# Kernel tuning notes

Hardware: AMD Instinct MI355X
Metric: run time of the kernel (lower is better)

## Reference

```python
import jax, jax.numpy as jnp
import numpy as np

EPS = 1e-4

def _softmax_kernel(x, proj, is_query):
    # x: [b,h,n,d], proj: [m,d]
    d = x.shape[-1]
    m = proj.shape[0]
    data_norm = 1.0 / d ** 0.25
    ratio = 1.0 / m ** 0.5
    xd = jnp.einsum('bhnd,md->bhnm', data_norm * x, proj)  # [b,h,n,m]
    diag = jnp.sum(x * x, axis=-1, keepdims=True) * (0.5 * data_norm ** 2)  # [b,h,n,1]
    if is_query:
        stab = jnp.max(xd, axis=-1, keepdims=True)  # per-row max
    else:
        stab = jnp.max(xd)  # global max, matches torch.max(data_dash)
    return ratio * (jnp.exp(xd - diag - stab) + EPS)

def setup_inputs() -> dict:
    key = jax.random.key(0)
    kq, kk, kv, kp = jax.random.split(key, 4)
    B, H, N, D, M = 4, 16, 4096, 64, 256
    return {
        'q': jax.random.normal(kq, (B, H, N, D), dtype=jnp.float32),
        'k': jax.random.normal(kk, (B, H, N, D), dtype=jnp.float32),
        'v': jax.random.normal(kv, (B, H, N, D), dtype=jnp.float32),
        'proj': jax.random.normal(kp, (M, D), dtype=jnp.float32),
    }

def reference(q, k, v, proj):
    q_kernel = _softmax_kernel(q, proj, is_query=True)   # [b,h,n,m]
    k_kernel = _softmax_kernel(k, proj, is_query=False)  # [b,h,n,m]
    context = jnp.einsum('bhnm,bhne->bhme', k_kernel, v)  # [b,h,m,e]
    out = jnp.einsum('bhme,bhnm->bhne', context, q_kernel)  # [b,h,n,e]
    return out
```

## Files before the change

kernel.cpp:

```cpp
#include <hip/hip_runtime.h>
#include <cstdint>

typedef __bf16 bf16x8 __attribute__((ext_vector_type(8)));
typedef float f32x16 __attribute__((ext_vector_type(16)));
typedef unsigned int u32;

#define MFMA32(a, b, c) __builtin_amdgcn_mfma_f32_32x32x16_bf16(a, b, c, 0, 0, 0)

static constexpr int NBH = 64;
static constexpr int NN  = 4096;
static constexpr int DD  = 64;
static constexpr int MM  = 256;
static constexpr float DATA_NORM = 0.35355339059327373f;
static constexpr float RATIO     = 0.0625f;
static constexpr float EPSK      = 1e-4f;

__device__ __forceinline__ unsigned short bfu(float f) {
  return __builtin_bit_cast(unsigned short, (__bf16)f);
}
__device__ __forceinline__ unsigned pk2(float a, float b) {
  return (unsigned)bfu(a) | ((unsigned)bfu(b) << 16);
}
__device__ __forceinline__ int vtByte(int ncb, int e) {
  const int wrap = e >> 3;
  const int grp = (e & 7) ^ (wrap & 7);
  return ncb * 1024 + wrap * 128 + grp * 16;
}
__device__ __forceinline__ void gload_lds4(const float* g, void* lds) {
  __builtin_amdgcn_global_load_lds((const __attribute__((address_space(1))) u32*)g,
                                   (__attribute__((address_space(3))) u32*)lds, 4, 0, 0);
}

__global__ void prep_proj(const float* __restrict__ proj, unsigned short* __restrict__ paU) {
  const int l = threadIdx.x, combo = blockIdx.x;
  const int mt = combo >> 2, kt = combo & 3;
  const int m = mt * 32 + (l & 31);
  const int d0 = kt * 16 + 8 * (l >> 5);
  unsigned short pk[8];
#pragma unroll
  for (int j = 0; j < 8; ++j) pk[j] = bfu(DATA_NORM * proj[m * 64 + d0 + j]);
  uint4 u = make_uint4(pk[0] | ((unsigned)pk[1] << 16), pk[2] | ((unsigned)pk[3] << 16),
                       pk[4] | ((unsigned)pk[5] << 16), pk[6] | ((unsigned)pk[7] << 16));
  *(uint4*)(paU + (size_t)(combo * 64 + l) * 8) = u;
}

__global__ __launch_bounds__(256, 3) void k_pass(
    const float* __restrict__ kk, const float* __restrict__ vv,
    const bf16x8* __restrict__ paG, float* __restrict__ s1p,
    float* __restrict__ s2p, unsigned* __restrict__ kmaxp, int NC) {
  __shared__ __align__(16) char smc[16896 + 8192];
  char* kbuf0 = smc;
  char* kbuf1 = smc + 8448;
  char* vbufB = smc + 16896;

  const int t = threadIdx.x, l = t & 63, wv = t >> 6;
  const int l31 = l & 31, lh = l >> 5;
  const int u = blockIdx.x;
  const int lin = (u >> 4) * 8 + (u & 7);
  const int ms = (u >> 3) & 1;
  const int bh = lin / NC, nc = lin - bh * NC;
  const int rowsPB = NN / NC, ntiles = rowsPB >> 5;
  const float* kb = kk + (size_t)bh * NN * DD;
  const float* vb = vv + (size_t)bh * NN * DD;
  const int base0 = nc * rowsPB;
  const int mslice = ms * 4 + wv;
  const bool doS2 = (ms == 0);
  const int ns = t >> 3, se0 = (t & 7) * 8;

  bf16x8 pb[4];
#pragma unroll
  for (int kt = 0; kt < 4; ++kt) pb[kt] = paG[(mslice * 4 + kt) * 64 + l];

  f32x16 accS[2];
#pragma unroll
  for (int et = 0; et < 2; ++et)
#pragma unroll
    for (int i = 0; i < 16; ++i) accS[et][i] = 0.f;
  float s2loc[8] = {0.f, 0.f, 0.f, 0.f, 0.f, 0.f, 0.f, 0.f};
  float gmax = -3.0e38f;

  float v8[8];
  bf16x8 KH[4];
  float nrm = 0.f;

#pragma unroll
  for (int i = 0; i < 8; ++i) {
    const int r = wv * 8 + i;
    gload_lds4(kb + (size_t)(base0 + r) * DD + l, kbuf0 + r * 264);
  }
  {
    const float* s = vb + (size_t)(base0 + ns) * DD + se0;
    *(float4*)&v8[0] = *(const float4*)s;
    *(float4*)&v8[4] = *(const float4*)(s + 4);
  }
  __syncthreads();
  {
    float ds = 0.f;
#pragma unroll
    for (int kt = 0; kt < 4; ++kt) {
      const char* p = kbuf0 + l31 * 264 + kt * 64 + lh * 32;
      float2 a = *(const float2*)(p);
      float2 b = *(const float2*)(p + 8);
      float2 c = *(const float2*)(p + 16);
      float2 d = *(const float2*)(p + 24);
      ds += a.x * a.x + a.y * a.y + b.x * b.x + b.y * b.y +
            c.x * c.x + c.y * c.y + d.x * d.x + d.y * d.y;
      KH[kt] = __builtin_bit_cast(bf16x8, make_uint4(pk2(a.x, a.y), pk2(b.x, b.y),
                                                     pk2(c.x, c.y), pk2(d.x, d.y)));
    }
    ds += __shfl_xor(ds, 32);
    nrm = ds * 0.0625f;
  }
  {
    const int ncb = ns >> 3, np2 = (ns & 7) * 2;
#pragma unroll
    for (int j = 0; j < 8; ++j) {
      s2loc[j] += v8[j];
      *(unsigned short*)(vbufB + vtByte(ncb, se0 + j) + np2) = bfu(v8[j]);
    }
  }
  if (ntiles > 1) {
#pragma unroll
    for (int i = 0; i < 8; ++i) {
      const int r = wv * 8 + i;
      gload_lds4(kb + (size_t)(base0 + 32 + r) * DD + l, kbuf1 + r * 264);
    }
    const float* s = vb + (size_t)(base0 + 32 + ns) * DD + se0;
    *(float4*)&v8[0] = *(const float4*)s;
    *(float4*)&v8[4] = *(const float4*)(s + 4);
  }
  __syncthreads();

  for (int tile = 0; tile < ntiles; ++tile) {
    if (tile + 1 < ntiles) {
      char* vtn = vbufB + ((tile + 1) & 1) * 4096;
      const int ncb = ns >> 3, np2 = (ns & 7) * 2;
#pragma unroll
      for (int j = 0; j < 8; ++j) {
        s2loc[j] += v8[j];
        *(unsigned short*)(vtn + vtByte(ncb, se0 + j) + np2) = bfu(v8[j]);
      }
    }
    if (tile + 2 < ntiles) {
      char* kdst = (tile & 1) ? kbuf1 : kbuf0;
      const int nb = base0 + (tile + 2) * 32;
#pragma unroll
      for (int i = 0; i < 8; ++i) {
        const int r = wv * 8 + i;
        gload_lds4(kb + (size_t)(nb + r) * DD + l, kdst + r * 264);
      }
      const float* s = vb + (size_t)(nb + ns) * DD + se0;
      *(float4*)&v8[0] = *(const float4*)s;
      *(float4*)&v8[4] = *(const float4*)(s + 4);
    }
    f32x16 acc;
#pragma unroll
    for (int i = 0; i < 16; ++i) acc[i] = 0.f;
#pragma unroll
    for (int kt = 0; kt < 4; ++kt) acc = MFMA32(KH[kt], pb[kt], acc);
#pragma unroll
    for (int i = 0; i < 16; ++i) gmax = fmaxf(gmax, acc[i]);
    {
      const char* vtc = vbufB + (tile & 1) * 4096;
#pragma unroll
      for (int kc = 0; kc < 2; ++kc) {
        float eA[4], eB[4];
#pragma unroll
        for (int c = 0; c < 4; ++c) {
          const float dgA = __shfl(nrm, kc * 16 + 4 * lh + c);
          const float dgB = __shfl(nrm, kc * 16 + 4 * lh + 8 + c);
          eA[c] = __expf(acc[kc * 8 + c] - dgA);
          eB[c] = __expf(acc[kc * 8 + 4 + c] - dgB);
        }
        unsigned p00 = pk2(eA[0], eA[1]), p01 = pk2(eA[2], eA[3]);
        unsigned p10 = pk2(eB[0], eB[1]), p11 = pk2(eB[2], eB[3]);
        unsigned o00 = __shfl_xor(p00, 32), o01 = __shfl_xor(p01, 32);
        unsigned o10 = __shfl_xor(p10, 32), o11 = __shfl_xor(p11, 32);
        uint4 W;
        W.x = lh ? o10 : p00;
        W.y = lh ? o11 : p01;
        W.z = lh ? p10 : o00;
        W.w = lh ? p11 : o01;
        bf16x8 af = __builtin_bit_cast(bf16x8, W);
#pragma unroll
        for (int et = 0; et < 2; ++et) {
          const int e = et * 32 + l31;
          bf16x8 bv = *(const bf16x8*)(vtc + vtByte(kc * 2 + lh, e));
          accS[et] = MFMA32(af, bv, accS[et]);
        }
      }
    }
    if (tile + 1 < ntiles) {
      const char* ksrc = ((tile + 1) & 1) ? kbuf1 : kbuf0;
      float ds = 0.f;
#pragma unroll
      for (int kt = 0; kt < 4; ++kt) {
        const char* p = ksrc + l31 * 264 + kt * 64 + lh * 32;
        float2 a = *(const float2*)(p);
        float2 b = *(const float2*)(p + 8);
        float2 c = *(const float2*)(p + 16);
        float2 d = *(const float2*)(p + 24);
        ds += a.x * a.x + a.y * a.y + b.x * b.x + b.y * b.y +
              c.x * c.x + c.y * c.y + d.x * d.x + d.y * d.y;
        KH[kt] = __builtin_bit_cast(bf16x8, make_uint4(pk2(a.x, a.y), pk2(b.x, b.y),
                                                       pk2(c.x, c.y), pk2(d.x, d.y)));
      }
      ds += __shfl_xor(ds, 32);
      nrm = ds * 0.0625f;
    }
    __syncthreads();
  }
  {
    float* o = s1p + (size_t)(bh * NC + nc) * (MM * 64);
#pragma unroll
    for (int et = 0; et < 2; ++et)
#pragma unroll
      for (int i = 0; i < 16; ++i) {
        const int m = mslice * 32 + 4 * lh + (i & 3) + 8 * (i >> 2);
        o[m * 64 + et * 32 + l31] = accS[et][i];
      }
  }
  {
    float* scr = (float*)smc;
#pragma unroll
    for (int j = 0; j < 8; ++j) scr[t * 8 + j] = s2loc[j];
    __syncthreads();
    if (doS2 && t < 64) {
      float s = 0.f;
      for (int k2 = 0; k2 < 32; ++k2) s += scr[((k2 << 3) | (t >> 3)) * 8 + (t & 7)];
      s2p[(size_t)(bh * NC + nc) * 64 + t] = s;
    }
  }
#pragma unroll
  for (int off = 32; off; off >>= 1) gmax = fmaxf(gmax, __shfl_xor(gmax, off));
  if (l == 0) {
    unsigned b = __float_as_uint(gmax);
    unsigned key = (b & 0x80000000u) ? ~b : (b | 0x80000000u);
    atomicMax(kmaxp, key);
  }
}

__global__ void ctx_finalize(const float* __restrict__ s1p, const float* __restrict__ s2p,
                             const unsigned* __restrict__ kmaxp, unsigned short* __restrict__ cbU,
                             float* __restrict__ epstP, int NC) {
  __shared__ float ctxl[16 * 64];
  __shared__ float s2s[64];
  __shared__ float csr[4 * 64];
  const int t = threadIdx.x;
  const int bh = blockIdx.x >> 4, gg = blockIdx.x & 15;
  const unsigned key = *kmaxp;
  const unsigned b = (key & 0x80000000u) ? (key & 0x7fffffffu) : ~key;
  const float stab = __uint_as_float(b);
  const float esc = RATIO * __expf(-stab);
  if (t < 64) {
    float s = 0.f;
    for (int nc = 0; nc < NC; ++nc) s += s2p[(size_t)(bh * NC + nc) * 64 + t];
    s2s[t] = RATIO * EPSK * s;
  }
  __syncthreads();
  const int e = t & 63, w = t >> 6;
  float cs = 0.f;
#pragma unroll
  for (int i = 0; i < 4; ++i) {
    const int ml = i * 4 + w;
    const int idx = (gg * 16 + ml) * 64 + e;
    float s = 0.f;
#pragma unroll
    for (int nc = 0; nc < 8; ++nc) s += s1p[(size_t)(bh * NC + nc) * 16384 + idx];
    const float val = esc * s + s2s[e];
    ctxl[ml * 64 + e] = val;
    cs += val;
  }
  csr[w * 64 + e] = cs;
  __syncthreads();
  if (t < 64)
    epstP[(size_t)(bh * 16 + gg) * 64 + t] =
        RATIO * EPSK * (csr[t] + csr[64 + t] + csr[128 + t] + csr[192 + t]);
  if (t < 128) {
    const int et = t >> 6, l = t & 63;
    unsigned short pk[8];
#pragma unroll
    for (int j = 0; j < 8; ++j) {
      const int ml = 8 * (l >> 5) + j;
      const int e2 = et * 32 + (l & 31);
      pk[j] = bfu(ctxl[ml * 64 + e2]);
    }
    uint4 u = make_uint4(pk[0] | ((unsigned)pk[1] << 16), pk[2] | ((unsigned)pk[3] << 16),
                         pk[4] | ((unsigned)pk[5] << 16), pk[6] | ((unsigned)pk[7] << 16));
    *(uint4*)(cbU + (size_t)bh * 16384 + (size_t)((gg * 2 + et) * 64 + l) * 8) = u;
  }
}

__global__ __launch_bounds__(256, 3) void q_pass(
    const float* __restrict__ qq, const bf16x8* __restrict__ paG,
    const bf16x8* __restrict__ cbG, const float* __restrict__ epstP,
    float* __restrict__ outp) {
  const int t = threadIdx.x, l = t & 63, wv = t >> 6;
  const int l31 = l & 31, lh = l >> 5;
  const int bid = blockIdx.x, bh = bid >> 5, nc = bid & 31;
  const float* qb = qq + (size_t)bh * NN * DD;
  float* ob = outp + (size_t)bh * NN * DD;
  const int base = nc * 128 + wv * 32;
  const bf16x8* cbB = cbG + (size_t)bh * 2048;

  float ept0 = 0.f, ept1 = 0.f;
#pragma unroll
  for (int g = 0; g < 16; ++g) {
    ept0 += epstP[(size_t)(bh * 16 + g) * 64 + l31];
    ept1 += epstP[(size_t)(bh * 16 + g) * 64 + 32 + l31];
  }

  bf16x8 QH[4];
  float ds = 0.f;
#pragma unroll
  for (int kt = 0; kt < 4; ++kt) {
    const float* p = qb + (size_t)(base + l31) * DD + kt * 16 + 8 * lh;
    float x[8];
    *(float4*)&x[0] = *(const float4*)p;
    *(float4*)&x[4] = *(const float4*)(p + 4);
#pragma unroll
    for (int j = 0; j < 8; ++j) ds += x[j] * x[j];
    QH[kt] = __builtin_bit_cast(bf16x8, make_uint4(pk2(x[0], x[1]), pk2(x[2], x[3]),
                                                   pk2(x[4], x[5]), pk2(x[6], x[7])));
  }
  ds += __shfl_xor(ds, 32);
  const float diag = ds * 0.0625f;

  f32x16 out0, out1;
#pragma unroll
  for (int i = 0; i < 16; ++i) { out0[i] = 0.f; out1[i] = 0.f; }
  float lmax = -3.0e38f;

  bf16x8 pa[4], cbv[4];
#pragma unroll
  for (int kt = 0; kt < 4; ++kt) pa[kt] = paG[kt * 64 + l];
#pragma unroll
  for (int j = 0; j < 4; ++j) cbv[j] = cbB[j * 64 + l];

  for (int mt = 0; mt < 8; ++mt) {
    f32x16 acc;
#pragma unroll
    for (int i = 0; i < 16; ++i) acc[i] = 0.f;
#pragma unroll
    for (int kt = 0; kt < 4; ++kt) acc = MFMA32(pa[kt], QH[kt], acc);
    bf16x8 pan[4], cbn[4];
    if (mt < 7) {
#pragma unroll
      for (int kt = 0; kt < 4; ++kt) pan[kt] = paG[((mt + 1) * 4 + kt) * 64 + l];
#pragma unroll
      for (int j = 0; j < 4; ++j) cbn[j] = cbB[((mt + 1) * 4 + j) * 64 + l];
    }
#pragma unroll
    for (int i = 0; i < 16; ++i) lmax = fmaxf(lmax, acc[i]);
#pragma unroll
    for (int kc = 0; kc < 2; ++kc) {
      float eA[4], eB[4];
#pragma unroll
      for (int c = 0; c < 4; ++c) {
        eA[c] = __expf(acc[kc * 8 + c] - diag);
        eB[c] = __expf(acc[kc * 8 + 4 + c] - diag);
      }
      unsigned p00 = pk2(eA[0], eA[1]), p01 = pk2(eA[2], eA[3]);
      unsigned p10 = pk2(eB[0], eB[1]), p11 = pk2(eB[2], eB[3]);
      unsigned o00 = __shfl_xor(p00, 32), o01 = __shfl_xor(p01, 32);
      unsigned o10 = __shfl_xor(p10, 32), o11 = __shfl_xor(p11, 32);
      uint4 W;
      W.x = lh ? o10 : p00;
      W.y = lh ? o11 : p01;
      W.z = lh ? p10 : o00;
      W.w = lh ? p11 : o01;
      bf16x8 af = __builtin_bit_cast(bf16x8, W);
      out0 = MFMA32(af, cbv[kc * 2 + 0], out0);
      out1 = MFMA32(af, cbv[kc * 2 + 1], out1);
    }
    if (mt < 7) {
#pragma unroll
      for (int kt = 0; kt < 4; ++kt) pa[kt] = pan[kt];
#pragma unroll
      for (int j = 0; j < 4; ++j) cbv[j] = cbn[j];
    }
  }
  const float rmaxp = fmaxf(lmax, __shfl_xor(lmax, 32));
#pragma unroll
  for (int i = 0; i < 16; ++i) {
    const int rr = 4 * lh + (i & 3) + 8 * (i >> 2);
    const float st = __shfl(rmaxp, rr);
    const float sc = RATIO * __expf(-st);
    const int row = base + rr;
    ob[(size_t)row * 64 + l31]      = sc * out0[i] + ept0;
    ob[(size_t)row * 64 + 32 + l31] = sc * out1[i] + ept1;
  }
}

extern "C" void kernel_launch(void* const* d_in, const int* in_sizes, int n_in,
                              void* d_out, int out_size, void* d_ws, size_t ws_size,
                              hipStream_t stream) {
  (void)in_sizes; (void)n_in; (void)out_size;
  const float* q    = (const float*)d_in[0];
  const float* k    = (const float*)d_in[1];
  const float* v    = (const float*)d_in[2];
  const float* proj = (const float*)d_in[3];
  float* out = (float*)d_out;
  char* wsb = (char*)d_ws;

  int NC = 8;
  auto need = [&](int nc) -> size_t {
    size_t off = 256 + 32768;
    off += (size_t)nc * NBH * MM * 64 * 4;
    off += (size_t)nc * NBH * 64 * 4;
    off += (size_t)NBH * MM * 64 * 2;
    off += (size_t)NBH * 16 * 64 * 4;
    return off;
  };
  while (NC > 1 && need(NC) > ws_size) NC >>= 1;

  unsigned* kmaxp = (unsigned*)wsb;
  bf16x8* paG = (bf16x8*)(wsb + 256);
  float* s1p = (float*)(wsb + 256 + 32768);
  float* s2p = (float*)((char*)s1p + (size_t)NC * NBH * MM * 64 * 4);
  unsigned short* cbU = (unsigned short*)((char*)s2p + (size_t)NC * NBH * 64 * 4);
  float* epstP = (float*)((char*)cbU + (size_t)NBH * MM * 64 * 2);

  hipMemsetAsync(wsb, 0, 4, stream);
  hipLaunchKernelGGL(prep_proj, dim3(32), dim3(64), 0, stream, proj, (unsigned short*)paG);
  hipLaunchKernelGGL(k_pass, dim3(NBH * NC * 2), dim3(256), 0, stream, k, v, paG, s1p, s2p, kmaxp, NC);
  hipLaunchKernelGGL(ctx_finalize, dim3(NBH * 16), dim3(256), 0, stream, s1p, s2p, kmaxp, cbU, epstP, NC);
  hipLaunchKernelGGL(q_pass, dim3(NBH * 32), dim3(256), 0, stream, q, paG, (const bf16x8*)cbU, epstP, out);
}
```

Measured before the change: 147.1 us.

## Stream V tiles into LDS via global_load_lds and convert to bf16 at use

V is no longer loaded into registers, transposed and converted to bf16 before being written to a swizzled LDS buffer. Raw fp32 V rows now go straight to LDS with asynchronous global_load_lds, double-buffered one tile ahead, and each lane reads its column values and packs them to bf16 just before the MFMA. The V column sum is accumulated by a single wave from those same reads, which replaces the LDS scratch reduction. The aim is to cut VGPR pressure and per-tile VALU and LDS-store work, at the cost of twice the LDS for V and strided 4-byte LDS reads that may bank-conflict.

```diff
diff --git a/kernel.cpp b/kernel.cpp
--- a/kernel.cpp
+++ b/kernel.cpp
@@ -21,11 +21,6 @@
 __device__ __forceinline__ unsigned pk2(float a, float b) {
   return (unsigned)bfu(a) | ((unsigned)bfu(b) << 16);
 }
-__device__ __forceinline__ int vtByte(int ncb, int e) {
-  const int wrap = e >> 3;
-  const int grp = (e & 7) ^ (wrap & 7);
-  return ncb * 1024 + wrap * 128 + grp * 16;
-}
 __device__ __forceinline__ void gload_lds4(const float* g, void* lds) {
   __builtin_amdgcn_global_load_lds((const __attribute__((address_space(1))) u32*)g,
                                    (__attribute__((address_space(3))) u32*)lds, 4, 0, 0);
@@ -48,7 +43,7 @@
     const float* __restrict__ kk, const float* __restrict__ vv,
     const bf16x8* __restrict__ paG, float* __restrict__ s1p,
     float* __restrict__ s2p, unsigned* __restrict__ kmaxp, int NC) {
-  __shared__ __align__(16) char smc[16896 + 8192];
+  __shared__ __align__(16) char smc[16896 + 16384];
   char* kbuf0 = smc;
   char* kbuf1 = smc + 8448;
   char* vbufB = smc + 16896;
@@ -64,8 +59,7 @@
   const float* vb = vv + (size_t)bh * NN * DD;
   const int base0 = nc * rowsPB;
   const int mslice = ms * 4 + wv;
-  const bool doS2 = (ms == 0);
-  const int ns = t >> 3, se0 = (t & 7) * 8;
+  const bool doS2 = (ms == 0) && (wv == 0);
 
   bf16x8 pb[4];
 #pragma unroll
@@ -76,10 +70,9 @@
   for (int et = 0; et < 2; ++et)
 #pragma unroll
     for (int i = 0; i < 16; ++i) accS[et][i] = 0.f;
-  float s2loc[8] = {0.f, 0.f, 0.f, 0.f, 0.f, 0.f, 0.f, 0.f};
+  float s2a0 = 0.f, s2a1 = 0.f;
   float gmax = -3.0e38f;
 
-  float v8[8];
   bf16x8 KH[4];
   float nrm = 0.f;
 
@@ -87,11 +80,7 @@
   for (int i = 0; i < 8; ++i) {
     const int r = wv * 8 + i;
     gload_lds4(kb + (size_t)(base0 + r) * DD + l, kbuf0 + r * 264);
-  }
-  {
-    const float* s = vb + (size_t)(base0 + ns) * DD + se0;
-    *(float4*)&v8[0] = *(const float4*)s;
-    *(float4*)&v8[4] = *(const float4*)(s + 4);
+    gload_lds4(vb + (size_t)(base0 + r) * DD + l, vbufB + r * 256);
   }
   __syncthreads();
   {
@@ -111,36 +100,16 @@
     ds += __shfl_xor(ds, 32);
     nrm = ds * 0.0625f;
   }
-  {
-    const int ncb = ns >> 3, np2 = (ns & 7) * 2;
-#pragma unroll
-    for (int j = 0; j < 8; ++j) {
-      s2loc[j] += v8[j];
-      *(unsigned short*)(vbufB + vtByte(ncb, se0 + j) + np2) = bfu(v8[j]);
-    }
-  }
   if (ntiles > 1) {
 #pragma unroll
     for (int i = 0; i < 8; ++i) {
       const int r = wv * 8 + i;
       gload_lds4(kb + (size_t)(base0 + 32 + r) * DD + l, kbuf1 + r * 264);
     }
-    const float* s = vb + (size_t)(base0 + 32 + ns) * DD + se0;
-    *(float4*)&v8[0] = *(const float4*)s;
-    *(float4*)&v8[4] = *(const float4*)(s + 4);
   }
   __syncthreads();
 
   for (int tile = 0; tile < ntiles; ++tile) {
-    if (tile + 1 < ntiles) {
-      char* vtn = vbufB + ((tile + 1) & 1) * 4096;
-      const int ncb = ns >> 3, np2 = (ns & 7) * 2;
-#pragma unroll
-      for (int j = 0; j < 8; ++j) {
-        s2loc[j] += v8[j];
-        *(unsigned short*)(vtn + vtByte(ncb, se0 + j) + np2) = bfu(v8[j]);
-      }
-    }
     if (tile + 2 < ntiles) {
       char* kdst = (tile & 1) ? kbuf1 : kbuf0;
       const int nb = base0 + (tile + 2) * 32;
@@ -149,9 +118,15 @@
         const int r = wv * 8 + i;
         gload_lds4(kb + (size_t)(nb + r) * DD + l, kdst + r * 264);
       }
-      const float* s = vb + (size_t)(nb + ns) * DD + se0;
-      *(float4*)&v8[0] = *(const float4*)s;
-      *(float4*)&v8[4] = *(const float4*)(s + 4);
+    }
+    if (tile + 1 < ntiles) {
+      char* vdst = vbufB + ((tile + 1) & 1) * 8192;
+      const int nb = base0 + (tile + 1) * 32;
+#pragma unroll
+      for (int i = 0; i < 8; ++i) {
+        const int r = wv * 8 + i;
+        gload_lds4(vb + (size_t)(nb + r) * DD + l, vdst + r * 256);
+      }
     }
     f32x16 acc;
 #pragma unroll
@@ -161,9 +136,16 @@
 #pragma unroll
     for (int i = 0; i < 16; ++i) gmax = fmaxf(gmax, acc[i]);
     {
-      const char* vtc = vbufB + (tile & 1) * 4096;
+      const char* vtc = vbufB + (tile & 1) * 8192;
 #pragma unroll
       for (int kc = 0; kc < 2; ++kc) {
+        const int rb = kc * 16 + 8 * lh;
+        float vf0[8], vf1[8];
+#pragma unroll
+        for (int j = 0; j < 8; ++j) {
+          vf0[j] = *(const float*)(vtc + (rb + j) * 256 + l31 * 4);
+          vf1[j] = *(const float*)(vtc + (rb + j) * 256 + (32 + l31) * 4);
+        }
         float eA[4], eB[4];
 #pragma unroll
         for (int c = 0; c < 4; ++c) {
@@ -182,12 +164,18 @@
         W.z = lh ? p10 : o00;
         W.w = lh ? p11 : o01;
         bf16x8 af = __builtin_bit_cast(bf16x8, W);
-#pragma unroll
-        for (int et = 0; et < 2; ++et) {
-          const int e = et * 32 + l31;
-          bf16x8 bv = *(const bf16x8*)(vtc + vtByte(kc * 2 + lh, e));
-          accS[et] = MFMA32(af, bv, accS[et]);
+        if (doS2) {
+#pragma unroll
+          for (int j = 0; j < 8; ++j) { s2a0 += vf0[j]; s2a1 += vf1[j]; }
         }
+        bf16x8 bv0 = __builtin_bit_cast(bf16x8,
+            make_uint4(pk2(vf0[0], vf0[1]), pk2(vf0[2], vf0[3]),
+                       pk2(vf0[4], vf0[5]), pk2(vf0[6], vf0[7])));
+        bf16x8 bv1 = __builtin_bit_cast(bf16x8,
+            make_uint4(pk2(vf1[0], vf1[1]), pk2(vf1[2], vf1[3]),
+                       pk2(vf1[4], vf1[5]), pk2(vf1[6], vf1[7])));
+        accS[0] = MFMA32(af, bv0, accS[0]);
+        accS[1] = MFMA32(af, bv1, accS[1]);
       }
     }
     if (tile + 1 < ntiles) {
@@ -220,15 +208,12 @@
         o[m * 64 + et * 32 + l31] = accS[et][i];
       }
   }
-  {
-    float* scr = (float*)smc;
-#pragma unroll
-    for (int j = 0; j < 8; ++j) scr[t * 8 + j] = s2loc[j];
-    __syncthreads();
-    if (doS2 && t < 64) {
-      float s = 0.f;
-      for (int k2 = 0; k2 < 32; ++k2) s += scr[((k2 << 3) | (t >> 3)) * 8 + (t & 7)];
-      s2p[(size_t)(bh * NC + nc) * 64 + t] = s;
+  if (doS2) {
+    s2a0 += __shfl_xor(s2a0, 32);
+    s2a1 += __shfl_xor(s2a1, 32);
+    if (lh == 0) {
+      s2p[(size_t)(bh * NC + nc) * 64 + l31]      = s2a0;
+      s2p[(size_t)(bh * NC + nc) * 64 + 32 + l31] = s2a1;
     }
   }
 #pragma unroll
```

Result: slower. 152.9 us (+4.0%).
